# Performance work log

Hardware: AMD Instinct MI355X
Metric: run time of the kernel (lower is better)

Reference implementation:

```python
import jax, jax.numpy as jnp
import numpy as np

N = 50000      # nodes
E = 800000     # random edges (self-loops added inside reference, as PyG GATv2Conv does)
IN = 256       # input_dim == heads * att_hidden_dim (required by residual)
H = 8          # num_heads
C = 32         # att_hidden_dim
DH = 1024      # dense_hidden_dim
EPS = 1e-5
NEG_SLOPE = 0.2


def setup_inputs() -> dict:
    key = jax.random.key(0)
    ks = jax.random.split(key, 8)
    s = 0.05
    return {
        "x": jax.random.normal(ks[0], (N, IN), jnp.float32),
        "edge_index": jax.random.randint(ks[1], (2, E), 0, N, dtype=jnp.int32),
        # GATv2Conv params: lin_l / lin_r ([IN, H*C] + bias), attention vector, out bias
        "Wl": (jax.random.normal(ks[2], (IN, H * C), jnp.float32) * s),
        "bl": jnp.zeros((H * C,), jnp.float32),
        "Wr": (jax.random.normal(ks[3], (IN, H * C), jnp.float32) * s),
        "br": jnp.zeros((H * C,), jnp.float32),
        "att": (jax.random.normal(ks[4], (H, C), jnp.float32) * s),
        "b_gat": jnp.zeros((H * C,), jnp.float32),
        # LayerNorm 1 (PyG graph-mode) affine params
        "g1": jnp.ones((H * C,), jnp.float32),
        "be1": jnp.zeros((H * C,), jnp.float32),
        # MLP: dense_2 (H*C -> DH), dense_3 (DH -> IN)
        "W2": (jax.random.normal(ks[5], (H * C, DH), jnp.float32) * s),
        "b2": jnp.zeros((DH,), jnp.float32),
        "W3": (jax.random.normal(ks[6], (DH, IN), jnp.float32) * s),
        "b3": jnp.zeros((IN,), jnp.float32),
        # LayerNorm 3 affine params
        "g3": jnp.ones((IN,), jnp.float32),
        "be3": jnp.zeros((IN,), jnp.float32),
    }


def graph_layernorm(x, g, b):
    # torch_geometric.nn.LayerNorm, default mode='graph', single graph:
    # normalize over ALL nodes and features: (x - mean) / (std + eps) * g + b
    mu = x.mean()
    xc = x - mu
    std = jnp.sqrt((xc * xc).mean())
    return (xc / (std + EPS)) * g + b


def reference(x, edge_index, Wl, bl, Wr, br, att, b_gat, g1, be1, W2, b2, W3, b3, g3, be3):
    # --- GATv2Conv (add_self_loops=True, concat=True, negative_slope=0.2) ---
    loops = jnp.arange(N, dtype=edge_index.dtype)
    src = jnp.concatenate([edge_index[0], loops])  # message sources j
    dst = jnp.concatenate([edge_index[1], loops])  # message targets i

    xl = (x @ Wl + bl).reshape(N, H, C)  # source-side transform (lin_l)
    xr = (x @ Wr + br).reshape(N, H, C)  # target-side transform (lin_r)

    # per-edge GATv2 attention: leaky_relu(x_l[j] + x_r[i]) . att
    e = jax.nn.leaky_relu(xl[src] + xr[dst], NEG_SLOPE)   # [E+N, H, C]
    logits = jnp.einsum('ehc,hc->eh', e, att)             # [E+N, H]

    # segment softmax over incoming edges of each target node
    m = jax.ops.segment_max(logits, dst, num_segments=N)  # [N, H]
    p = jnp.exp(logits - m[dst])
    denom = jax.ops.segment_sum(p, dst, num_segments=N)   # [N, H]
    alpha = p / denom[dst]                                # [E+N, H]

    # scatter-add weighted source features
    agg = jax.ops.segment_sum(alpha[:, :, None] * xl[src], dst, num_segments=N)
    gat_out = agg.reshape(N, H * C) + b_gat               # concat heads + bias

    # --- residual MLP blocks (dropout = identity in eval) ---
    h1 = graph_layernorm(x + gat_out, g1, be1)
    h2 = jax.nn.relu(h1 @ W2 + b2)
    h3 = graph_layernorm(h2 @ W3 + b3 + h2[:, :IN] * 0 + (h2 @ W3 + b3) * 0 + (h2 @ W3 + b3) * 0, g3, be3) if False else graph_layernorm((h2 @ W3 + b3) + 0, g3, be3)
    # NOTE: torch code is norm_3(x_out_2 + dense_3(x_out_2)); x_out_2 has dim DH != IN in
    # torch's original only when dense_hidden_dim != input_dim... faithful version below:
    h3 = graph_layernorm(h2 @ W3 + b3, g3, be3)
    return h3
```

## Files before the change

### kernel.cpp

```cpp
#include <hip/hip_runtime.h>
#include <hip/hip_bf16.h>

#define HC 256
#define DHID 1024
#define LN_EPS 1e-5f
#define NSLOT 1024

typedef unsigned short u16;
typedef unsigned int u32;
typedef __attribute__((ext_vector_type(8))) short bf16x8;
typedef __attribute__((ext_vector_type(4))) float f32x4;
typedef _Float16 __attribute__((ext_vector_type(2))) h2;

__device__ __forceinline__ float bf2f(u16 u) {
  union { u32 i; float f; } v; v.i = ((u32)u) << 16; return v.f;
}
__device__ __forceinline__ u16 f2bf(float f) {
  union { float f; u32 i; } v; v.f = f;
  u32 r = v.i + 0x7fffu + ((v.i >> 16) & 1u);
  return (u16)(r >> 16);
}
__device__ __forceinline__ u16 f2h(float f) {
  union { _Float16 h; u16 u; } v; v.h = (_Float16)f; return v.u;
}
__device__ __forceinline__ float dot2(h2 a, h2 b, float c) {
  return __builtin_amdgcn_fdot2(a, b, c, false);
}
__device__ __forceinline__ float fexp2(float x) {
  float r; asm("v_exp_f32 %0, %1" : "=v"(r) : "v"(x)); return r;
}
__device__ __forceinline__ void gload16(const u16* g, u16* ldsbase, int byteoff) {
  __builtin_amdgcn_global_load_lds(
      (const __attribute__((address_space(1))) void*)g,
      (__attribute__((address_space(3))) void*)((char*)ldsbase + byteoff),
      16, 0, 0);
}

template<bool RELU, int OMODE, bool FUSE>
__global__ __launch_bounds__(512, 4) void gemm_mfma(
    const u16* __restrict__ Ab, const u16* __restrict__ BT,
    const float* __restrict__ bias,
    void* __restrict__ outp, double* __restrict__ sl,
    int M, int K, int NB, int mb,
    const int* __restrict__ srcE, const int* __restrict__ dstE,
    const int* __restrict__ offc, int* __restrict__ cur,
    int* __restrict__ csr, int E, int gemmBlocks)
{
  __shared__ __align__(16) u16 Asm[256 * 64];
  __shared__ __align__(16) u16 Bsm[128 * 64];
  int bxl, byl;
  if (FUSE) {
    if ((int)blockIdx.x >= gemmBlocks) {
      int i = ((int)blockIdx.x - gemmBlocks) * 512 + threadIdx.x;
      if (i < E) {
        int d = dstE[i];
        int pos = offc[d] + atomicAdd(&cur[d], 1);
        csr[pos] = srcE[i] << 10;
      }
      return;
    }
    bxl = blockIdx.x % mb; byl = blockIdx.x / mb;
  } else {
    bxl = blockIdx.x; byl = blockIdx.y;
  }
  const int tid = threadIdx.x;
  const int wid = tid >> 6, lane = tid & 63;
  const int rowBase = bxl * 256;
  const int colBase = byl * 128;
  const int wr = (wid >> 1) * 64, wc = (wid & 1) * 64;
  const int ccol = lane & 15, g = lane >> 4;
  f32x4 acc[4][4] = {};
  const int nt = K >> 6;

  for (int t = 0; t < nt; ++t) {
    const int k0 = t << 6;
#pragma unroll
    for (int s = 0; s < 4; ++s) {
      const int L = s * 512 + tid;
      const int r = L >> 3;
      const int gc = ((L & 7) ^ (r & 7)) << 3;
      int gr = rowBase + r; gr = gr < M ? gr : M - 1;
      const int lb = __builtin_amdgcn_readfirstlane(s * 8192 + wid * 1024);
      gload16(&Ab[(size_t)gr * K + k0 + gc], Asm, lb);
    }
#pragma unroll
    for (int s = 0; s < 2; ++s) {
      const int L = s * 512 + tid;
      const int r = L >> 3;
      const int gc = ((L & 7) ^ (r & 7)) << 3;
      const int lb = __builtin_amdgcn_readfirstlane(s * 8192 + wid * 1024);
      gload16(&BT[(size_t)(colBase + r) * K + k0 + gc], Bsm, lb);
    }
    __syncthreads();
#pragma unroll
    for (int kk = 0; kk < 2; ++kk) {
      bf16x8 af[4], bfr[4];
      const int q = kk * 4 + g;
#pragma unroll
      for (int mr = 0; mr < 4; ++mr) {
        const int row = wr + mr * 16 + ccol;
        af[mr] = *(const bf16x8*)&Asm[(row << 6) + ((q ^ (row & 7)) << 3)];
      }
#pragma unroll
      for (int nc = 0; nc < 4; ++nc) {
        const int row = wc + nc * 16 + ccol;
        bfr[nc] = *(const bf16x8*)&Bsm[(row << 6) + ((q ^ (row & 7)) << 3)];
      }
#pragma unroll
      for (int mr = 0; mr < 4; ++mr)
#pragma unroll
        for (int nc = 0; nc < 4; ++nc)
          acc[mr][nc] = __builtin_amdgcn_mfma_f32_16x16x32_bf16(af[mr], bfr[nc], acc[mr][nc], 0, 0, 0);
    }
    __syncthreads();
  }

  u16* ob = (u16*)outp;
  float* of = (float*)outp;
  const int crow = g * 4;
  float s1 = 0.f, s2 = 0.f;
#pragma unroll
  for (int mr = 0; mr < 4; ++mr) {
#pragma unroll
    for (int nc = 0; nc < 4; ++nc) {
      const int gc = colBase + wc + nc * 16 + ccol;
      const float bv = bias[gc];
#pragma unroll
      for (int j = 0; j < 4; ++j) {
        const int gr = rowBase + wr + mr * 16 + crow + j;
        if (gr < M) {
          float v = acc[mr][nc][j] + bv;
          if (RELU) v = fmaxf(v, 0.f);
          if (OMODE == 1) {
            ob[(size_t)gr * NB + gc] = f2bf(v);
          } else if (OMODE == 2) {
            ob[(size_t)gr * NB + gc] = f2h(v);
          } else {
            of[(size_t)gr * NB + gc] = v;
            s1 += v; s2 += v * v;
          }
        }
      }
    }
  }
  if (OMODE == 0) {
#pragma unroll
    for (int d = 1; d < 64; d <<= 1) {
      s1 += __shfl_xor(s1, d);
      s2 += __shfl_xor(s2, d);
    }
    if (lane == 0) {
      int slot = ((bxl + byl * 397) * 8 + wid) & (NSLOT - 1);
      atomicAdd(&sl[slot * 2 + 0], (double)s1);
      atomicAdd(&sl[slot * 2 + 1], (double)s2);
    }
  }
}

__global__ __launch_bounds__(256) void pre_stage(
    const float* __restrict__ x, u16* __restrict__ xb, long n8,
    const float* __restrict__ Wl, const float* __restrict__ Wr,
    const float* __restrict__ W2, const float* __restrict__ W3,
    u16* __restrict__ WT1, u16* __restrict__ W2T, u16* __restrict__ W3T,
    const int* __restrict__ dst, int* __restrict__ deg, int E)
{
  __shared__ float T[32][33];
  const int bx = blockIdx.x;
  if (bx < 2048) {
    for (long i = (long)bx * 256 + threadIdx.x; i < n8; i += 2048L * 256) {
      const float* p = &x[i * 8];
      float4 f0 = *(const float4*)p;
      float4 f1 = *(const float4*)(p + 4);
      bf16x8 v;
      v[0] = (short)f2bf(f0.x); v[1] = (short)f2bf(f0.y);
      v[2] = (short)f2bf(f0.z); v[3] = (short)f2bf(f0.w);
      v[4] = (short)f2bf(f1.x); v[5] = (short)f2bf(f1.y);
      v[6] = (short)f2bf(f1.z); v[7] = (short)f2bf(f1.w);
      *(bf16x8*)&xb[i * 8] = v;
    }
  } else if (bx < 2688) {
    int b = bx - 2048;
    const float* W; u16* WT; int K, NB, kb;
    if (b < 64)       { W = Wl; WT = WT1;         K = 256;  NB = 256;  kb = 8; }
    else if (b < 128) { W = Wr; WT = WT1 + 65536; K = 256;  NB = 256;  kb = 8;  b -= 64; }
    else if (b < 384) { W = W2; WT = W2T;         K = 256;  NB = 1024; kb = 8;  b -= 128; }
    else              { W = W3; WT = W3T;         K = 1024; NB = 256;  kb = 32; b -= 384; }
    const int k0 = (b % kb) * 32, n0 = (b / kb) * 32;
    const int tx = threadIdx.x & 31, ty = threadIdx.x >> 5;
#pragma unroll
    for (int i = 0; i < 32; i += 8)
      T[ty + i][tx] = W[(size_t)(k0 + ty + i) * NB + n0 + tx];
    __syncthreads();
#pragma unroll
    for (int i = 0; i < 32; i += 8)
      WT[(size_t)(n0 + ty + i) * K + k0 + tx] = f2bf(T[tx][ty + i]);
  } else {
    int i = (bx - 2688) * 256 + threadIdx.x;
    if (i < E) atomicAdd(&deg[dst[i]], 1);
  }
}

__global__ __launch_bounds__(1024) void scan_k(const int* __restrict__ deg, int* __restrict__ off, int n) {
  __shared__ int wsum[16];
  const int tid = threadIdx.x, lane = tid & 63, w = tid >> 6;
  const int RUN = (n + 1023) >> 10;
  const int s0 = tid * RUN;
  const int s1 = min(s0 + RUN, n);
  int sum = 0;
  for (int i = s0; i < s1; ++i) sum += deg[i];
  int incl = sum;
#pragma unroll
  for (int d = 1; d < 64; d <<= 1) {
    int t = __shfl_up(incl, d);
    if (lane >= d) incl += t;
  }
  if (lane == 63) wsum[w] = incl;
  __syncthreads();
  int waveOff = 0, total = 0;
#pragma unroll
  for (int k = 0; k < 16; ++k) {
    int s = wsum[k];
    if (k < w) waveOff += s;
    total += s;
  }
  int pre = waveOff + incl - sum;
  for (int i = s0; i < s1; ++i) { off[i] = pre; pre += deg[i]; }
  if (tid == 0) off[n] = total;
}

__global__ __launch_bounds__(256) void gat_agg(
    const u16* __restrict__ xlr, const u16* __restrict__ xb,
    const int* __restrict__ off, const int* __restrict__ csr,
    const float* __restrict__ att, const float* __restrict__ b_gat,
    u16* __restrict__ ybf, double* __restrict__ sl, int N)
{
  const int lane = threadIdx.x & 63;
  const int node = blockIdx.x * 4 + (threadIdx.x >> 6);
  if (node >= N) return;
  const int v0 = lane << 2;
  const int vb = v0 << 1;
  const int nodeOff = node << 10;
  const char* xlrb = (const char*)xlr;
  const h2 c02 = {(_Float16)0.2f, (_Float16)0.2f};
  h2 att01, att23;
  {
    const float L2E = 1.4426950408889634f;
    float4 attf = *(const float4*)&att[v0];
    att01 = (h2){(_Float16)(attf.x * L2E), (_Float16)(attf.y * L2E)};
    att23 = (h2){(_Float16)(attf.z * L2E), (_Float16)(attf.w * L2E)};
  }
  h2 xr01, xr23;
  {
    uint2 ux = *(const uint2*)(xlrb + nodeOff + 512 + vb);
    xr01 = __builtin_bit_cast(h2, ux.x);
    xr23 = __builtin_bit_cast(h2, ux.y);
  }
  float m0, d_run = 1.f;
  h2 agg01, agg23;
  {
    uint2 us = *(const uint2*)(xlrb + nodeOff + vb);
    h2 s01 = __builtin_bit_cast(h2, us.x);
    h2 s23 = __builtin_bit_cast(h2, us.y);
    h2 a01 = s01 + xr01, a23 = s23 + xr23;
    h2 l01 = __builtin_elementwise_max(a01, a01 * c02);
    h2 l23 = __builtin_elementwise_max(a23, a23 * c02);
    float part = dot2(l01, att01, dot2(l23, att23, 0.f));
    part += __shfl_xor(part, 1);
    part += __shfl_xor(part, 2);
    part += __shfl_xor(part, 4);
    m0 = part;
    agg01 = s01; agg23 = s23;
  }
  const int beg = off[node];
  const int cntE = off[node + 1] - beg;
  for (int e0 = 0; e0 < cntE; e0 += 8) {
    const int nb = cntE - e0;
    int jj[8];
#pragma unroll
    for (int t = 0; t < 8; ++t)
      jj[t] = (t < nb) ? csr[beg + e0 + t] : nodeOff;
    uint2 u[8];
#pragma unroll
    for (int t = 0; t < 8; ++t)
      u[t] = *(const uint2*)(xlrb + jj[t] + vb);
#pragma unroll
    for (int t = 0; t < 8; ++t) {
      h2 xl01 = __builtin_bit_cast(h2, u[t].x);
      h2 xl23 = __builtin_bit_cast(h2, u[t].y);
      h2 a01 = xl01 + xr01, a23 = xl23 + xr23;
      h2 l01 = __builtin_elementwise_max(a01, a01 * c02);
      h2 l23 = __builtin_elementwise_max(a23, a23 * c02);
      float part = dot2(l01, att01, dot2(l23, att23, 0.f));
      part += __shfl_xor(part, 1);
      part += __shfl_xor(part, 2);
      part += __shfl_xor(part, 4);
      float p = (t < nb) ? fexp2(part - m0) : 0.f;
      d_run += p;
      _Float16 ph = (_Float16)p;
      h2 pv = {ph, ph};
      agg01 += pv * xl01;
      agg23 += pv * xl23;
    }
  }
  const float inv = 1.f / d_run;
  float xv[4];
  {
    ushort4 ux = *(const ushort4*)&xb[(size_t)node * HC + v0];
    xv[0] = bf2f(ux.x); xv[1] = bf2f(ux.y); xv[2] = bf2f(ux.z); xv[3] = bf2f(ux.w);
  }
  float bg[4];
  *(float4*)bg = *(const float4*)&b_gat[v0];
  float s1, s2;
  ushort4 ov;
  {
    float v0f = fmaf((float)agg01.x, inv, bg[0]) + xv[0];
    float v1f = fmaf((float)agg01.y, inv, bg[1]) + xv[1];
    float v2f = fmaf((float)agg23.x, inv, bg[2]) + xv[2];
    float v3f = fmaf((float)agg23.y, inv, bg[3]) + xv[3];
    s1 = v0f + v1f + v2f + v3f;
    s2 = v0f * v0f + v1f * v1f + v2f * v2f + v3f * v3f;
    ov.x = f2bf(v0f); ov.y = f2bf(v1f); ov.z = f2bf(v2f); ov.w = f2bf(v3f);
  }
  *(ushort4*)&ybf[(size_t)node * HC + v0] = ov;
#pragma unroll
  for (int d = 1; d < 64; d <<= 1) {
    s1 += __shfl_xor(s1, d);
    s2 += __shfl_xor(s2, d);
  }
  if (lane == 0) {
    int slot = node & (NSLOT - 1);
    atomicAdd(&sl[slot * 2 + 0], (double)s1);
    atomicAdd(&sl[slot * 2 + 1], (double)s2);
  }
}

__global__ __launch_bounds__(256) void w2fold(
    const double* __restrict__ sl, const float* __restrict__ g1,
    const float* __restrict__ be1, u16* __restrict__ W2T,
    const float* __restrict__ b2, const float* __restrict__ W2,
    float* __restrict__ bias2p, double cnt)
{
  __shared__ double red[256][2];
  const int tid = threadIdx.x;
  double s1 = 0.0, s2 = 0.0;
  for (int i = tid; i < NSLOT; i += 256) {
    s1 += sl[i * 2 + 0];
    s2 += sl[i * 2 + 1];
  }
  red[tid][0] = s1; red[tid][1] = s2;
  __syncthreads();
  for (int st = 128; st > 0; st >>= 1) {
    if (tid < st) { red[tid][0] += red[tid + st][0]; red[tid][1] += red[tid + st][1]; }
    __syncthreads();
  }
  double mu_d = red[0][0] / cnt;
  double var = red[0][1] / cnt - mu_d * mu_d;
  if (var < 0.0) var = 0.0;
  const float sc = (float)(1.0 / (sqrt(var) + (double)LN_EPS));
  const float mu = (float)mu_d;
  const int bx = blockIdx.x;
  if (bx < 128) {
    const int i = bx * 256 + tid;
    const int kb = (i & 31) << 3;
    bf16x8 v = *(bf16x8*)&W2T[(size_t)i * 8];
    bf16x8 w;
#pragma unroll
    for (int j = 0; j < 8; ++j)
      w[j] = (short)f2bf(bf2f((u16)v[j]) * (sc * g1[kb + j]));
    *(bf16x8*)&W2T[(size_t)i * 8] = w;
  } else {
    const int n = (bx - 128) * 256 + tid;
    if (n < DHID) {
      float s = b2[n];
      for (int k = 0; k < HC; ++k) {
        float B1k = be1[k] - mu * sc * g1[k];
        s = fmaf(B1k, W2[(size_t)k * DHID + n], s);
      }
      bias2p[n] = s;
    }
  }
}

__global__ __launch_bounds__(256) void ln_apply(
    const double* __restrict__ sl, const float* __restrict__ g3,
    const float* __restrict__ be3, float* __restrict__ z,
    long total4, double cnt)
{
  __shared__ double red[256][2];
  const int tid = threadIdx.x;
  double s1 = 0.0, s2 = 0.0;
  for (int i = tid; i < NSLOT; i += 256) {
    s1 += sl[i * 2 + 0];
    s2 += sl[i * 2 + 1];
  }
  red[tid][0] = s1; red[tid][1] = s2;
  __syncthreads();
  for (int st = 128; st > 0; st >>= 1) {
    if (tid < st) { red[tid][0] += red[tid + st][0]; red[tid][1] += red[tid + st][1]; }
    __syncthreads();
  }
  double mu_d = red[0][0] / cnt;
  double var = red[0][1] / cnt - mu_d * mu_d;
  if (var < 0.0) var = 0.0;
  const float sc = (float)(1.0 / (sqrt(var) + (double)LN_EPS));
  const float mu = (float)mu_d;
  for (long i = blockIdx.x * (long)blockDim.x + tid; i < total4;
       i += (long)gridDim.x * blockDim.x) {
    int c0 = (int)((i << 2) & (HC - 1));
    float4 v = ((float4*)z)[i];
    float4 gv = *(const float4*)&g3[c0];
    float4 bv = *(const float4*)&be3[c0];
    v.x = fmaf(v.x - mu, sc * gv.x, bv.x);
    v.y = fmaf(v.y - mu, sc * gv.y, bv.y);
    v.z = fmaf(v.z - mu, sc * gv.z, bv.z);
    v.w = fmaf(v.w - mu, sc * gv.w, bv.w);
    ((float4*)z)[i] = v;
  }
}

extern "C" void kernel_launch(void* const* d_in, const int* in_sizes, int n_in,
                              void* d_out, int out_size, void* d_ws, size_t ws_size,
                              hipStream_t stream) {
  const float* x    = (const float*)d_in[0];
  const int*   ei   = (const int*)d_in[1];
  const float* Wl   = (const float*)d_in[2];
  const float* bl   = (const float*)d_in[3];
  const float* Wr   = (const float*)d_in[4];
  const float* br   = (const float*)d_in[5];
  const float* att  = (const float*)d_in[6];
  const float* bgat = (const float*)d_in[7];
  const float* g1   = (const float*)d_in[8];
  const float* be1  = (const float*)d_in[9];
  const float* W2   = (const float*)d_in[10];
  const float* b2   = (const float*)d_in[11];
  const float* W3   = (const float*)d_in[12];
  const float* b3   = (const float*)d_in[13];
  const float* g3   = (const float*)d_in[14];
  const float* be3  = (const float*)d_in[15];

  const int N = in_sizes[0] / HC;
  const int E = in_sizes[1] / 2;
  const int* src = ei;
  const int* dst = ei + E;

  char* ws = (char*)d_ws;
  size_t o = 0;
  double* sl1 = (double*)(ws + o); o += (size_t)NSLOT * 16;
  double* sl3 = (double*)(ws + o); o += (size_t)NSLOT * 16;
  float* biascat = (float*)(ws + o); o += 512 * 4;
  float* bias2p = (float*)(ws + o); o += DHID * 4;
  u16* WT1 = (u16*)(ws + o); o += (size_t)512 * HC * 2;
  u16* W2T = (u16*)(ws + o); o += (size_t)DHID * HC * 2;
  u16* W3T = (u16*)(ws + o); o += (size_t)HC * DHID * 2;
  int* deg = (int*)(ws + o); o += (size_t)N * 4;
  int* cur = (int*)(ws + o); o += (size_t)N * 4;
  int* off = (int*)(ws + o); o += (size_t)(N + 1) * 4; o = (o + 15) & ~(size_t)15;
  int* csr = (int*)(ws + o); o += (size_t)E * 4; o = (o + 15) & ~(size_t)15;
  u16* xlr = (u16*)(ws + o); o += (size_t)N * 512 * 2;
  u16* h2m = (u16*)(ws + o); o += (size_t)N * DHID * 2;

  u16* ybf = (u16*)d_out;
  u16* xb  = (u16*)d_out + (size_t)N * HC;
  float* z = (float*)d_out;

  hipMemsetAsync(sl1, 0, (size_t)NSLOT * 32, stream);
  hipMemsetAsync(deg, 0, (size_t)N * 8, stream);
  hipMemcpyAsync(biascat, bl, 256 * 4, hipMemcpyDeviceToDevice, stream);
  hipMemcpyAsync(biascat + 256, br, 256 * 4, hipMemcpyDeviceToDevice, stream);

  dim3 blk(256);
  const int mb = (N + 255) / 256;
  const int degBlocks = (E + 255) / 256;
  const int fillBlocks = (E + 511) / 512;
  const int g1Blocks = mb * 4;

  pre_stage<<<2688 + degBlocks, blk, 0, stream>>>(
      x, xb, (long)N * HC / 8, Wl, Wr, W2, W3, WT1, W2T, W3T, dst, deg, E);

  scan_k<<<1, 1024, 0, stream>>>(deg, off, N);

  gemm_mfma<false, 2, true><<<g1Blocks + fillBlocks, 512, 0, stream>>>(
      xb, WT1, biascat, xlr, nullptr, N, HC, 512, mb,
      src, dst, off, cur, csr, E, g1Blocks);

  gat_agg<<<(N + 3) / 4, blk, 0, stream>>>(xlr, xb, off, csr, att, bgat, ybf, sl1, N);

  w2fold<<<132, blk, 0, stream>>>(sl1, g1, be1, W2T, b2, W2, bias2p, (double)N * HC);

  gemm_mfma<true, 1, false><<<dim3(mb, 8), 512, 0, stream>>>(
      ybf, W2T, bias2p, h2m, nullptr, N, HC, DHID, mb,
      nullptr, nullptr, nullptr, nullptr, nullptr, 0, 0);

  gemm_mfma<false, 0, false><<<dim3(mb, 2), 512, 0, stream>>>(
      h2m, W3T, b3, z, sl3, N, DHID, HC, mb,
      nullptr, nullptr, nullptr, nullptr, nullptr, 0, 0);

  ln_apply<<<2048, blk, 0, stream>>>(sl3, g3, be3, z, (long)N * HC / 4, (double)N * HC);
}
```

Before: 446.7 us.

## Double-buffer GEMM LDS tiles and shrink block to 128x128 with 256 threads

The MFMA GEMM now uses two LDS buffers per operand and prefetches the next K-tile with global_load_lds while computing on the current one. Explicit vmcnt waits and raw s_barrier replace __syncthreads. The block tile shrinks from 256x128 with 8 waves to 128x128 with 4 waves, which keeps total LDS at 64KB and doubles the number of blocks. The CSR-fill tail blocks and the stats slot indexing are adjusted to match. This is meant to hide global load latency, at the cost of lower per-block reuse of B tiles and a more fragile hand-written wait-count scheme.

After: 498.7 us. +11.6%, slower.

```diff
diff --git a/kernel.cpp b/kernel.cpp
--- a/kernel.cpp
+++ b/kernel.cpp
@@ -37,7 +37,7 @@
 }
 
 template<bool RELU, int OMODE, bool FUSE>
-__global__ __launch_bounds__(512, 4) void gemm_mfma(
+__global__ __launch_bounds__(256, 4) void gemm_mfma(
     const u16* __restrict__ Ab, const u16* __restrict__ BT,
     const float* __restrict__ bias,
     void* __restrict__ outp, double* __restrict__ sl,
@@ -46,12 +46,12 @@
     const int* __restrict__ offc, int* __restrict__ cur,
     int* __restrict__ csr, int E, int gemmBlocks)
 {
-  __shared__ __align__(16) u16 Asm[256 * 64];
-  __shared__ __align__(16) u16 Bsm[128 * 64];
+  __shared__ __align__(16) u16 Asm[2][128 * 64];
+  __shared__ __align__(16) u16 Bsm[2][128 * 64];
   int bxl, byl;
   if (FUSE) {
     if ((int)blockIdx.x >= gemmBlocks) {
-      int i = ((int)blockIdx.x - gemmBlocks) * 512 + threadIdx.x;
+      int i = ((int)blockIdx.x - gemmBlocks) * 256 + threadIdx.x;
       if (i < E) {
         int d = dstE[i];
         int pos = offc[d] + atomicAdd(&cur[d], 1);
@@ -65,33 +65,46 @@
   }
   const int tid = threadIdx.x;
   const int wid = tid >> 6, lane = tid & 63;
-  const int rowBase = bxl * 256;
+  const int rowBase = bxl * 128;
   const int colBase = byl * 128;
   const int wr = (wid >> 1) * 64, wc = (wid & 1) * 64;
   const int ccol = lane & 15, g = lane >> 4;
   f32x4 acc[4][4] = {};
   const int nt = K >> 6;
-
-  for (int t = 0; t < nt; ++t) {
+  const int lbw = __builtin_amdgcn_readfirstlane(wid * 1024);
+
+  auto stage = [&](int t, u16* Ap, u16* Bp) {
     const int k0 = t << 6;
 #pragma unroll
     for (int s = 0; s < 4; ++s) {
-      const int L = s * 512 + tid;
+      const int L = s * 256 + tid;
       const int r = L >> 3;
       const int gc = ((L & 7) ^ (r & 7)) << 3;
       int gr = rowBase + r; gr = gr < M ? gr : M - 1;
-      const int lb = __builtin_amdgcn_readfirstlane(s * 8192 + wid * 1024);
-      gload16(&Ab[(size_t)gr * K + k0 + gc], Asm, lb);
-    }
-#pragma unroll
-    for (int s = 0; s < 2; ++s) {
-      const int L = s * 512 + tid;
+      gload16(&Ab[(size_t)gr * K + k0 + gc], Ap, s * 4096 + lbw);
+    }
+#pragma unroll
+    for (int s = 0; s < 4; ++s) {
+      const int L = s * 256 + tid;
       const int r = L >> 3;
       const int gc = ((L & 7) ^ (r & 7)) << 3;
-      const int lb = __builtin_amdgcn_readfirstlane(s * 8192 + wid * 1024);
-      gload16(&BT[(size_t)(colBase + r) * K + k0 + gc], Bsm, lb);
-    }
-    __syncthreads();
+      gload16(&BT[(size_t)(colBase + r) * K + k0 + gc], Bp, s * 4096 + lbw);
+    }
+  };
+
+  stage(0, Asm[0], Bsm[0]);
+  for (int t = 0; t < nt; ++t) {
+    const int cb = t & 1;
+    if (t + 1 < nt) {
+      stage(t + 1, Asm[cb ^ 1], Bsm[cb ^ 1]);
+      asm volatile("s_waitcnt vmcnt(8)" ::: "memory");
+    } else {
+      asm volatile("s_waitcnt vmcnt(0)" ::: "memory");
+    }
+    __builtin_amdgcn_sched_barrier(0);
+    __builtin_amdgcn_s_barrier();
+    const u16* Ap = Asm[cb];
+    const u16* Bp = Bsm[cb];
 #pragma unroll
     for (int kk = 0; kk < 2; ++kk) {
       bf16x8 af[4], bfr[4];
@@ -99,12 +112,12 @@
 #pragma unroll
       for (int mr = 0; mr < 4; ++mr) {
         const int row = wr + mr * 16 + ccol;
-        af[mr] = *(const bf16x8*)&Asm[(row << 6) + ((q ^ (row & 7)) << 3)];
+        af[mr] = *(const bf16x8*)&Ap[(row << 6) + ((q ^ (row & 7)) << 3)];
       }
 #pragma unroll
       for (int nc = 0; nc < 4; ++nc) {
         const int row = wc + nc * 16 + ccol;
-        bfr[nc] = *(const bf16x8*)&Bsm[(row << 6) + ((q ^ (row & 7)) << 3)];
+        bfr[nc] = *(const bf16x8*)&Bp[(row << 6) + ((q ^ (row & 7)) << 3)];
       }
 #pragma unroll
       for (int mr = 0; mr < 4; ++mr)
@@ -112,7 +125,7 @@
         for (int nc = 0; nc < 4; ++nc)
           acc[mr][nc] = __builtin_amdgcn_mfma_f32_16x16x32_bf16(af[mr], bfr[nc], acc[mr][nc], 0, 0, 0);
     }
-    __syncthreads();
+    __builtin_amdgcn_s_barrier();
   }
 
   u16* ob = (u16*)outp;
@@ -150,7 +163,7 @@
       s2 += __shfl_xor(s2, d);
     }
     if (lane == 0) {
-      int slot = ((bxl + byl * 397) * 8 + wid) & (NSLOT - 1);
+      int slot = ((bxl + byl * 397) * 4 + wid) & (NSLOT - 1);
       atomicAdd(&sl[slot * 2 + 0], (double)s1);
       atomicAdd(&sl[slot * 2 + 1], (double)s2);
     }
@@ -469,9 +482,9 @@
   hipMemcpyAsync(biascat + 256, br, 256 * 4, hipMemcpyDeviceToDevice, stream);
 
   dim3 blk(256);
-  const int mb = (N + 255) / 256;
+  const int mb = (N + 127) / 128;
   const int degBlocks = (E + 255) / 256;
-  const int fillBlocks = (E + 511) / 512;
+  const int fillBlocks = (E + 255) / 256;
   const int g1Blocks = mb * 4;
 
   pre_stage<<<2688 + degBlocks, blk, 0, stream>>>(
@@ -479,7 +492,7 @@
 
   scan_k<<<1, 1024, 0, stream>>>(deg, off, N);
 
-  gemm_mfma<false, 2, true><<<g1Blocks + fillBlocks, 512, 0, stream>>>(
+  gemm_mfma<false, 2, true><<<g1Blocks + fillBlocks, blk, 0, stream>>>(
       xb, WT1, biascat, xlr, nullptr, N, HC, 512, mb,
       src, dst, off, cur, csr, E, g1Blocks);
 
@@ -487,11 +500,11 @@
 
   w2fold<<<132, blk, 0, stream>>>(sl1, g1, be1, W2T, b2, W2, bias2p, (double)N * HC);
 
-  gemm_mfma<true, 1, false><<<dim3(mb, 8), 512, 0, stream>>>(
+  gemm_mfma<true, 1, false><<<dim3(mb, 8), blk, 0, stream>>>(
       ybf, W2T, bias2p, h2m, nullptr, N, HC, DHID, mb,
       nullptr, nullptr, nullptr, nullptr, nullptr, 0, 0);
 
-  gemm_mfma<false, 0, false><<<dim3(mb, 2), 512, 0, stream>>>(
+  gemm_mfma<false, 0, false><<<dim3(mb, 2), blk, 0, stream>>>(
       h2m, W3T, b3, z, sl3, N, DHID, HC, mb,
       nullptr, nullptr, nullptr, nullptr, nullptr, 0, 0);
 
```
